# Optimization experiments

Measured on AMD Instinct MI355X. Metric: run time of the kernel, lower is better.

The kernel has to match this reference:

```python
import jax, jax.numpy as jnp
import numpy as np

N, IN_DIM, OUT_DIM, BASIS = 262144, 128, 256, 7

def setup_inputs() -> dict:
    key = jax.random.key(0)
    k1, k2, k3, k4, k5 = jax.random.split(key, 5)
    return {
        "x": jax.random.normal(k1, (N, IN_DIM), dtype=jnp.float32),
        "W_s": jax.random.normal(k2, (IN_DIM, BASIS), dtype=jnp.float32) * (1.0 / np.sqrt(IN_DIM)),
        "b_s": jax.random.normal(k3, (BASIS,), dtype=jnp.float32) * 0.01,
        "W_m": jax.random.normal(k4, (2 * BASIS, 1), dtype=jnp.float32) * (1.0 / np.sqrt(2 * BASIS)),
        "b_m": jax.random.normal(k5, (1,), dtype=jnp.float32) * 0.01,
    }

def reference(x, W_s, b_s, W_m, b_m):
    # Fmap: linear -> [sin, cos] -> linear(->1)
    h = x @ W_s + b_s                                  # [N, basis]
    feats = jnp.concatenate((jnp.sin(h), jnp.cos(h)), axis=-1)  # [N, 2*basis]
    y = feats @ W_m + b_m                              # [N, 1]
    # Original uses `[Fmap(...)] * out_dim`: the SAME module repeated, so all
    # out_dim output columns are identical -> tile the single column.
    return jnp.broadcast_to(y, (y.shape[0], OUT_DIM))  # [N, out_dim]
```

## Files before the change

### kernel.cpp

```cpp
#include <hip/hip_runtime.h>

#define N_ROWS  262144
#define IN_DIM  128
#define OUT_DIM 256
#define BASIS   7

#define GRID    2048
#define BLOCK   256
#define NWAVES  ((GRID * BLOCK) / 64)
#define ITERS   (N_ROWS / (NWAVES * 4))

typedef float f4 __attribute__((ext_vector_type(4)));

__global__ __launch_bounds__(BLOCK) void flinear_kernel(
    const float* __restrict__ x,
    const float* __restrict__ W_s,
    const float* __restrict__ b_s,
    const float* __restrict__ W_m,
    const float* __restrict__ b_m,
    float* __restrict__ out)
{
    const int tid  = blockIdx.x * blockDim.x + threadIdx.x;
    const int wave = tid >> 6;
    const int lane = threadIdx.x & 63;
    const int sub  = lane & 15;
    const int grp  = lane >> 4;

    float w0[4][BASIS], w1[4][BASIS];
    #pragma unroll
    for (int e = 0; e < 4; ++e) {
        #pragma unroll
        for (int j = 0; j < BASIS; ++j) {
            w0[e][j] = W_s[(sub * 4 + e) * BASIS + j];
            w1[e][j] = W_s[(64 + sub * 4 + e) * BASIS + j];
        }
    }
    float bs[BASIS], wm_s[BASIS], wm_c[BASIS];
    #pragma unroll
    for (int j = 0; j < BASIS; ++j) {
        bs[j]   = b_s[j];
        wm_s[j] = W_m[j];
        wm_c[j] = W_m[BASIS + j];
    }
    const float bm = b_m[0];

    const int rowStride = NWAVES * 4;

    int rowBase = wave * 4;
    const float* xp = x + (rowBase + grp) * IN_DIM + sub * 4;

    f4 xa = __builtin_nontemporal_load(reinterpret_cast<const f4*>(xp));
    f4 xb = __builtin_nontemporal_load(reinterpret_cast<const f4*>(xp + 64));

    #pragma unroll
    for (int i = 0; i < ITERS; ++i) {
        f4 na = xa, nb = xb;
        if (i + 1 < ITERS) {
            const float* np = xp + rowStride * IN_DIM;
            na = __builtin_nontemporal_load(reinterpret_cast<const f4*>(np));
            nb = __builtin_nontemporal_load(reinterpret_cast<const f4*>(np + 64));
        }

        float h[BASIS];
        #pragma unroll
        for (int j = 0; j < BASIS; ++j) {
            h[j] = xa.x * w0[0][j] + xa.y * w0[1][j] + xa.z * w0[2][j] + xa.w * w0[3][j]
                 + xb.x * w1[0][j] + xb.y * w1[1][j] + xb.z * w1[2][j] + xb.w * w1[3][j];
        }

        #pragma unroll
        for (int m = 1; m < 16; m <<= 1) {
            #pragma unroll
            for (int j = 0; j < BASIS; ++j)
                h[j] += __shfl_xor(h[j], m, 64);
        }

        float y = bm;
        #pragma unroll
        for (int j = 0; j < BASIS; ++j) {
            float s, c;
            __sincosf(h[j] + bs[j], &s, &c);
            y += s * wm_s[j] + c * wm_c[j];
        }

        #pragma unroll
        for (int k = 0; k < 4; ++k) {
            const float yk = __shfl(y, k << 4, 64);
            f4 v = { yk, yk, yk, yk };
            f4* o = reinterpret_cast<f4*>(out + (size_t)(rowBase + k) * OUT_DIM) + lane;
            __builtin_nontemporal_store(v, o);
        }

        xp      += rowStride * IN_DIM;
        rowBase += rowStride;
        xa = na; xb = nb;
    }
}

extern "C" void kernel_launch(void* const* d_in, const int* in_sizes, int n_in,
                              void* d_out, int out_size, void* d_ws, size_t ws_size,
                              hipStream_t stream) {
    const float* x   = (const float*)d_in[0];
    const float* W_s = (const float*)d_in[1];
    const float* b_s = (const float*)d_in[2];
    const float* W_m = (const float*)d_in[3];
    const float* b_m = (const float*)d_in[4];
    float* out = (float*)d_out;

    flinear_kernel<<<GRID, BLOCK, 0, stream>>>(x, W_s, b_s, W_m, b_m, out);
}
```

Baseline: 75.56 us.

## Halve grid and deepen x prefetch to two iterations ahead

```diff
diff --git a/kernel.cpp b/kernel.cpp
--- a/kernel.cpp
+++ b/kernel.cpp
@@ -5,14 +5,14 @@
 #define OUT_DIM 256
 #define BASIS   7
 
-#define GRID    2048
+#define GRID    1024
 #define BLOCK   256
 #define NWAVES  ((GRID * BLOCK) / 64)
 #define ITERS   (N_ROWS / (NWAVES * 4))
 
 typedef float f4 __attribute__((ext_vector_type(4)));
 
-__global__ __launch_bounds__(BLOCK) void flinear_kernel(
+__global__ __launch_bounds__(BLOCK, 4) void flinear_kernel(
     const float* __restrict__ x,
     const float* __restrict__ W_s,
     const float* __restrict__ b_s,
@@ -44,28 +44,31 @@
     }
     const float bm = b_m[0];
 
-    const int rowStride = NWAVES * 4;
+    const int    rowStride = NWAVES * 4;
+    const size_t step      = (size_t)rowStride * IN_DIM;
 
     int rowBase = wave * 4;
-    const float* xp = x + (rowBase + grp) * IN_DIM + sub * 4;
+    const float* xp = x + (size_t)(rowBase + grp) * IN_DIM + sub * 4;
 
-    f4 xa = __builtin_nontemporal_load(reinterpret_cast<const f4*>(xp));
-    f4 xb = __builtin_nontemporal_load(reinterpret_cast<const f4*>(xp + 64));
+    f4 a0 = __builtin_nontemporal_load(reinterpret_cast<const f4*>(xp));
+    f4 b0 = __builtin_nontemporal_load(reinterpret_cast<const f4*>(xp + 64));
+    f4 a1 = __builtin_nontemporal_load(reinterpret_cast<const f4*>(xp + step));
+    f4 b1 = __builtin_nontemporal_load(reinterpret_cast<const f4*>(xp + step + 64));
 
-    #pragma unroll
+    #pragma unroll 2
     for (int i = 0; i < ITERS; ++i) {
-        f4 na = xa, nb = xb;
-        if (i + 1 < ITERS) {
-            const float* np = xp + rowStride * IN_DIM;
-            na = __builtin_nontemporal_load(reinterpret_cast<const f4*>(np));
-            nb = __builtin_nontemporal_load(reinterpret_cast<const f4*>(np + 64));
+        f4 a2 = a0, b2 = b0;
+        if (i + 2 < ITERS) {
+            const float* np = xp + 2 * step;
+            a2 = __builtin_nontemporal_load(reinterpret_cast<const f4*>(np));
+            b2 = __builtin_nontemporal_load(reinterpret_cast<const f4*>(np + 64));
         }
 
         float h[BASIS];
         #pragma unroll
         for (int j = 0; j < BASIS; ++j) {
-            h[j] = xa.x * w0[0][j] + xa.y * w0[1][j] + xa.z * w0[2][j] + xa.w * w0[3][j]
-                 + xb.x * w1[0][j] + xb.y * w1[1][j] + xb.z * w1[2][j] + xb.w * w1[3][j];
+            h[j] = a0.x * w0[0][j] + a0.y * w0[1][j] + a0.z * w0[2][j] + a0.w * w0[3][j]
+                 + b0.x * w1[0][j] + b0.y * w1[1][j] + b0.z * w1[2][j] + b0.w * w1[3][j];
         }
 
         #pragma unroll
@@ -91,9 +94,10 @@
             __builtin_nontemporal_store(v, o);
         }
 
-        xp      += rowStride * IN_DIM;
+        xp      += step;
         rowBase += rowStride;
-        xa = na; xb = nb;
+        a0 = a1; b0 = b1;
+        a1 = a2; b1 = b2;
     }
 }
 
```

Result: no change. 75.13 us (-0.6%).
